# Performance work log

Hardware: AMD Instinct MI355X
Metric: run time of the kernel (lower is better)

## Reference

```python
import jax, jax.numpy as jnp
import numpy as np


def conv3d(x, w, b=None):
    # x: (N,C,D,H,W), w: (O,I,3,3,3), stride 1, padding 1 == SAME
    y = jax.lax.conv_general_dilated(x, w, (1, 1, 1), 'SAME',
                                     dimension_numbers=('NCDHW', 'OIDHW', 'NCDHW'))
    if b is not None:
        y = y + b[None, :, None, None, None]
    return y


def grid_sample_3d(vol, gx, gy, gz):
    # vol: (B,D,H,W); gx/gy/gz: normalized coords in [-1,1], shape (B,D,H,W)
    # trilinear, zeros padding, align_corners=True (old torch default)
    B, D, H, W = vol.shape
    ix = (gx + 1.0) * 0.5 * (W - 1)
    iy = (gy + 1.0) * 0.5 * (H - 1)
    iz = (gz + 1.0) * 0.5 * (D - 1)
    x0f, y0f, z0f = jnp.floor(ix), jnp.floor(iy), jnp.floor(iz)
    tx, ty, tz = ix - x0f, iy - y0f, iz - z0f
    x0 = x0f.astype(jnp.int32)
    y0 = y0f.astype(jnp.int32)
    z0 = z0f.astype(jnp.int32)
    vol_flat = vol.reshape(B, D * H * W)
    out = jnp.zeros_like(vol)
    for dz in (0, 1):
        for dy in (0, 1):
            for dx in (0, 1):
                xc, yc, zc = x0 + dx, y0 + dy, z0 + dz
                w = ((tx if dx else 1.0 - tx) * (ty if dy else 1.0 - ty)
                     * (tz if dz else 1.0 - tz))
                inb = ((xc >= 0) & (xc < W) & (yc >= 0) & (yc < H)
                       & (zc >= 0) & (zc < D))
                idx = ((jnp.clip(zc, 0, D - 1) * H + jnp.clip(yc, 0, H - 1)) * W
                       + jnp.clip(xc, 0, W - 1))
                val = jnp.take_along_axis(vol_flat, idx.reshape(B, -1), axis=1)
                val = val.reshape(B, D, H, W) * inb.astype(vol.dtype)
                out = out + w * val
    return out


def setup_inputs() -> dict:
    key = jax.random.key(0)
    k1, k2, k3, k4 = jax.random.split(key, 4)
    B, C, Cout, S = 2, 32, 64, 64
    x = jax.random.normal(k1, (B, C, S, S, S), dtype=jnp.float32)
    w_off = jax.random.normal(k2, (3 * C, C, 3, 3, 3), dtype=jnp.float32) * 0.0005
    w_reg = jax.random.normal(k3, (Cout, C, 3, 3, 3), dtype=jnp.float32) * 0.05
    b_reg = jax.random.normal(k4, (Cout,), dtype=jnp.float32) * 0.05
    return {"x": x, "w_off": w_off, "w_reg": w_reg, "b_reg": b_reg}


def reference(x, w_off, w_reg, b_reg):
    B, C, D, H, W = x.shape
    offset = conv3d(x, w_off)  # (B, 3C, D, H, W)
    off_w, off_h, _ = jnp.split(offset, 3, axis=1)
    # NOTE: original code has offset_d = offset_h (faithful bug)
    off_d = off_h
    off_w = off_w.reshape(B * C, D, H, W)
    off_h = off_h.reshape(B * C, D, H, W)
    off_d = off_d.reshape(B * C, D, H, W)
    # np.meshgrid default 'xy' indexing: shapes (H, W, D) -> requires D==H==W
    gw, gh, gd = np.meshgrid(np.linspace(-1, 1, W), np.linspace(-1, 1, H),
                             np.linspace(-1, 1, D))
    grid_w = jnp.asarray(gw, dtype=x.dtype)
    grid_h = jnp.asarray(gh, dtype=x.dtype)
    grid_d = jnp.asarray(gd, dtype=x.dtype)
    off_w = off_w + grid_w
    off_h = off_h + grid_h
    off_d = off_d + grid_d
    vol = x.reshape(B * C, D, H, W)
    # torch grid stack order: (offset_h, offset_w, offset_d) -> (x, y, z)
    sampled = grid_sample_3d(vol, off_h, off_w, off_d)
    sampled = sampled.reshape(B, C, D, H, W)
    return conv3d(sampled, w_reg, b_reg)
```

## Files before the change

### kernel.cpp

```cpp
#include <hip/hip_runtime.h>
#include <cstddef>

#define S 64
#define VOL (64*64*64)
#define CIN 32

typedef __attribute__((ext_vector_type(8))) short bf16x8;
typedef __attribute__((ext_vector_type(4))) float floatx4;

__device__ __forceinline__ unsigned short f2bf(float f) {
    union { float f; unsigned u; } v; v.f = f;
    unsigned r = v.u + 0x7fffu + ((v.u >> 16) & 1u);
    return (unsigned short)(r >> 16);
}
__device__ __forceinline__ float bf2f(unsigned short h) {
    union { unsigned u; float f; } v; v.u = ((unsigned)h) << 16;
    return v.f;
}
__device__ __forceinline__ int iclamp(int v, int lo, int hi) {
    return v < lo ? lo : (v > hi ? hi : v);
}

__device__ __forceinline__ void load4bf(const float* p, unsigned short* o) {
    const float4 v = *(const float4*)p;
    o[0] = f2bf(v.x); o[1] = f2bf(v.y); o[2] = f2bf(v.z); o[3] = f2bf(v.w);
}
__device__ __forceinline__ void load4bf(const unsigned short* p, unsigned short* o) {
    const ushort4 v = *(const ushort4*)p;
    o[0] = v.x; o[1] = v.y; o[2] = v.z; o[3] = v.w;
}

__global__ void prep_w_kernel(const float* __restrict__ w_off,
                              const float* __restrict__ w_reg,
                              unsigned short* __restrict__ wt1,
                              unsigned short* __restrict__ wt2) {
    int i = blockIdx.x * 256 + threadIdx.x;
    if (i >= 27 * 64 * 32) return;
    int ci = i & 31;
    int co = (i >> 5) & 63;
    int tap = i >> 11;
    wt1[i] = f2bf(w_off[(co * 32 + ci) * 27 + tap]);
    wt2[i] = f2bf(w_reg[(co * 32 + ci) * 27 + tap]);
}

template <typename TIN, bool WRITE_BF16>
__global__ __launch_bounds__(256, 2)
void conv_mfma_kernel(const TIN* __restrict__ src,
                      const unsigned short* __restrict__ wt,
                      const float* __restrict__ bias,
                      void* __restrict__ dstv) {
    __shared__ unsigned short lds[16 * 64 * 32];

    const int d0 = blockIdx.x * 2;
    const int h0 = blockIdx.y * 2;
    const int b  = blockIdx.z;
    const int t  = threadIdx.x;

    const TIN* sb = src + (size_t)b * CIN * VOL;

    const int w0 = (t & 15) << 2;
    const int c0 = (t >> 4) << 1;
    const int jj = c0 >> 3;
    const int cb = (c0 & 7) << 1;
    const int sw01 = (w0 >> 1) & 3;
    const int sw23 = ((w0 >> 1) + 1) & 3;

#pragma unroll
    for (int rr = 0; rr < 16; ++rr) {
        const int z = d0 - 1 + (rr >> 2);
        const int y = h0 - 1 + (rr & 3);
        unsigned pk0 = 0, pk1 = 0, pk2 = 0, pk3 = 0;
        if (((unsigned)z < 64u) && ((unsigned)y < 64u)) {
            const TIN* p0 = sb + (size_t)c0 * VOL + (z * 64 + y) * 64 + w0;
            unsigned short va[4], vb[4];
            load4bf(p0, va);
            load4bf(p0 + VOL, vb);
            pk0 = (unsigned)va[0] | ((unsigned)vb[0] << 16);
            pk1 = (unsigned)va[1] | ((unsigned)vb[1] << 16);
            pk2 = (unsigned)va[2] | ((unsigned)vb[2] << 16);
            pk3 = (unsigned)va[3] | ((unsigned)vb[3] << 16);
        }
        char* rbase = (char*)lds + (rr << 12) + cb;
        *(unsigned*)(rbase + ((w0 + 0) << 6) + ((jj ^ sw01) << 4)) = pk0;
        *(unsigned*)(rbase + ((w0 + 1) << 6) + ((jj ^ sw01) << 4)) = pk1;
        *(unsigned*)(rbase + ((w0 + 2) << 6) + ((jj ^ sw23) << 4)) = pk2;
        *(unsigned*)(rbase + ((w0 + 3) << 6) + ((jj ^ sw23) << 4)) = pk3;
    }
    __syncthreads();

    const int lane = t & 63;
    const int wv   = t >> 6;
    const int r    = lane & 15;
    const int q    = lane >> 4;
    const int dd   = wv >> 1;
    const int hh   = wv & 1;

    int P[4][3];
#pragma unroll
    for (int nt = 0; nt < 4; ++nt)
#pragma unroll
        for (int kw = 0; kw < 3; ++kw) {
            const int s  = nt * 16 + r + kw - 1;
            const int sc = s & 63;
            P[nt][kw] = (sc << 6) + ((q ^ ((sc >> 1) & 3)) << 4);
        }

    floatx4 acc[4][4];
#pragma unroll
    for (int mt = 0; mt < 4; ++mt)
#pragma unroll
        for (int nt = 0; nt < 4; ++nt)
#pragma unroll
            for (int rg = 0; rg < 4; ++rg) acc[mt][nt][rg] = 0.f;

    const bf16x8 z8 = {0, 0, 0, 0, 0, 0, 0, 0};

#pragma unroll
    for (int tap = 0; tap < 27; ++tap) {
        const int kd = tap / 9;
        const int kh = (tap % 9) / 3;
        const int kw = tap % 3;
        const int rowb = ((((dd + kd) << 2) + hh + kh) << 12);

        bf16x8 afr[4];
#pragma unroll
        for (int mt = 0; mt < 4; ++mt)
            afr[mt] = *(const bf16x8*)&wt[tap * 2048 + (mt * 16 + r) * 32 + q * 8];

        bf16x8 bfr[4];
#pragma unroll
        for (int nt = 0; nt < 4; ++nt)
            bfr[nt] = *(const bf16x8*)((const char*)lds + rowb + P[nt][kw]);

        if (kw == 0) { if (r == 0)  bfr[0] = z8; }
        if (kw == 2) { if (r == 15) bfr[3] = z8; }

#pragma unroll
        for (int mt = 0; mt < 4; ++mt)
#pragma unroll
            for (int nt = 0; nt < 4; ++nt)
                acc[mt][nt] = __builtin_amdgcn_mfma_f32_16x16x32_bf16(
                                  afr[mt], bfr[nt], acc[mt][nt], 0, 0, 0);
    }

    const int dw = (d0 + dd) * 4096 + (h0 + hh) * 64;
#pragma unroll
    for (int mt = 0; mt < 4; ++mt) {
#pragma unroll
        for (int nt = 0; nt < 4; ++nt) {
#pragma unroll
            for (int rg = 0; rg < 4; ++rg) {
                const int co  = mt * 16 + q * 4 + rg;
                const int pos = dw + nt * 16 + r;
                const size_t oidx = ((size_t)(b * 64 + co)) * VOL + pos;
                const float v = acc[mt][nt][rg];
                if (WRITE_BF16) {
                    ((unsigned short*)dstv)[oidx] = f2bf(v);
                } else {
                    ((float*)dstv)[oidx] = v + bias[co];
                }
            }
        }
    }
}

__global__ __launch_bounds__(256)
void gather_kernel(const float* __restrict__ x,
                   const unsigned short* __restrict__ off,
                   unsigned short* __restrict__ sampled) {
    __shared__ float res[16][17];

    const int bx = blockIdx.x;
    const int wt4 = bx & 3;
    const int dt  = (bx >> 2) & 3;
    const int h   = bx >> 4;
    const int c = blockIdx.y;
    const int b = blockIdx.z;
    const int t = threadIdx.x;
    const int d_i = t & 15;
    const int w_i = t >> 4;
    const int d = dt * 16 + d_i;
    const int w = wt4 * 16 + w_i;
    const int p = d * 4096 + h * 64 + w;

    const float* vol = x + ((size_t)(b * CIN + c)) * VOL;
    const float offw = bf2f(off[((size_t)(b * 64 + c)) * VOL + p]);
    const float offh = bf2f(off[((size_t)(b * 64 + 32 + c)) * VOL + p]);

    const float ix = offh * 31.5f + (float)d;
    const float iy = offw * 31.5f + (float)h;
    const float iz = offh * 31.5f + (float)w;

    const float x0f = floorf(ix), y0f = floorf(iy), z0f = floorf(iz);
    const float tx = ix - x0f, ty = iy - y0f, tz = iz - z0f;
    const int ix0 = (int)x0f, iy0 = (int)y0f, iz0 = (int)z0f;

    float out = 0.f;
#pragma unroll
    for (int dz = 0; dz < 2; ++dz) {
#pragma unroll
        for (int dy = 0; dy < 2; ++dy) {
#pragma unroll
            for (int dx = 0; dx < 2; ++dx) {
                const int xc = ix0 + dx, yc = iy0 + dy, zc = iz0 + dz;
                const bool inb = ((unsigned)xc < 64u) && ((unsigned)yc < 64u)
                              && ((unsigned)zc < 64u);
                const float wgt = (dx ? tx : 1.f - tx)
                                * (dy ? ty : 1.f - ty)
                                * (dz ? tz : 1.f - tz);
                const int xcc = iclamp(xc, 0, 63);
                const int ycc = iclamp(yc, 0, 63);
                const int zcc = iclamp(zc, 0, 63);
                const float val = vol[(zcc * 64 + ycc) * 64 + xcc];
                out += inb ? wgt * val : 0.f;
            }
        }
    }

    res[w_i][d_i] = out;
    __syncthreads();

    const int w_o = t & 15;
    const int d_o = t >> 4;
    sampled[((size_t)(b * CIN + c)) * VOL + (dt * 16 + d_o) * 4096 + h * 64
            + wt4 * 16 + w_o] = f2bf(res[w_o][d_o]);
}

extern "C" void kernel_launch(void* const* d_in, const int* in_sizes, int n_in,
                              void* d_out, int out_size, void* d_ws, size_t ws_size,
                              hipStream_t stream) {
    (void)in_sizes; (void)n_in; (void)out_size; (void)ws_size;
    const float* x     = (const float*)d_in[0];
    const float* w_off = (const float*)d_in[1];
    const float* w_reg = (const float*)d_in[2];
    const float* b_reg = (const float*)d_in[3];
    float* out = (float*)d_out;

    unsigned short* off     = (unsigned short*)d_ws;
    unsigned short* sampled = off + (size_t)2 * 64 * VOL;
    unsigned short* wt1     = sampled + (size_t)2 * CIN * VOL;
    unsigned short* wt2     = wt1 + 27 * 64 * 32;

    prep_w_kernel<<<216, 256, 0, stream>>>(w_off, w_reg, wt1, wt2);

    dim3 cgrid(32, 32, 2);
    conv_mfma_kernel<float, true><<<cgrid, 256, 0, stream>>>(x, wt1, nullptr, (void*)off);

    dim3 ggrid(1024, 32, 2);
    gather_kernel<<<ggrid, 256, 0, stream>>>(x, off, sampled);

    conv_mfma_kernel<unsigned short, false><<<cgrid, 256, 0, stream>>>(sampled, wt2, b_reg, (void*)out);
}
```

Measured before the change: 467.4 us.

## Pack offset pairs, remap gather grid per XCD, and load x-neighbors as pairs

Measured after the change: 426.2 us. -8.8%, faster.

```diff
diff --git a/kernel.cpp b/kernel.cpp
--- a/kernel.cpp
+++ b/kernel.cpp
@@ -7,6 +7,8 @@
 
 typedef __attribute__((ext_vector_type(8))) short bf16x8;
 typedef __attribute__((ext_vector_type(4))) float floatx4;
+
+struct __attribute__((packed, aligned(4))) fpair { float x, y; };
 
 __device__ __forceinline__ unsigned short f2bf(float f) {
     union { float f; unsigned u; } v; v.f = f;
@@ -43,7 +45,7 @@
     wt2[i] = f2bf(w_reg[(co * 32 + ci) * 27 + tap]);
 }
 
-template <typename TIN, bool WRITE_BF16>
+template <typename TIN, bool WRITE_OFF>
 __global__ __launch_bounds__(256, 2)
 void conv_mfma_kernel(const TIN* __restrict__ src,
                       const unsigned short* __restrict__ wt,
@@ -144,48 +146,74 @@
     }
 
     const int dw = (d0 + dd) * 4096 + (h0 + hh) * 64;
-#pragma unroll
-    for (int mt = 0; mt < 4; ++mt) {
-#pragma unroll
-        for (int nt = 0; nt < 4; ++nt) {
-#pragma unroll
-            for (int rg = 0; rg < 4; ++rg) {
-                const int co  = mt * 16 + q * 4 + rg;
-                const int pos = dw + nt * 16 + r;
-                const size_t oidx = ((size_t)(b * 64 + co)) * VOL + pos;
-                const float v = acc[mt][nt][rg];
-                if (WRITE_BF16) {
-                    ((unsigned short*)dstv)[oidx] = f2bf(v);
-                } else {
-                    ((float*)dstv)[oidx] = v + bias[co];
+    if (WRITE_OFF) {
+#pragma unroll
+        for (int mt = 0; mt < 2; ++mt) {
+#pragma unroll
+            for (int nt = 0; nt < 4; ++nt) {
+#pragma unroll
+                for (int rg = 0; rg < 4; ++rg) {
+                    const int c   = mt * 16 + q * 4 + rg;
+                    const int pos = dw + nt * 16 + r;
+                    const unsigned pk = (unsigned)f2bf(acc[mt][nt][rg])
+                                      | ((unsigned)f2bf(acc[mt + 2][nt][rg]) << 16);
+                    ((unsigned*)dstv)[((size_t)(b * 32 + c)) * VOL + pos] = pk;
                 }
             }
         }
+    } else {
+#pragma unroll
+        for (int mt = 0; mt < 4; ++mt) {
+#pragma unroll
+            for (int nt = 0; nt < 4; ++nt) {
+#pragma unroll
+                for (int rg = 0; rg < 4; ++rg) {
+                    const int co  = mt * 16 + q * 4 + rg;
+                    const int pos = dw + nt * 16 + r;
+                    ((float*)dstv)[((size_t)(b * 64 + co)) * VOL + pos]
+                        = acc[mt][nt][rg] + bias[co];
+                }
+            }
+        }
     }
 }
 
 __global__ __launch_bounds__(256)
 void gather_kernel(const float* __restrict__ x,
-                   const unsigned short* __restrict__ off,
+                   const unsigned* __restrict__ off32,
                    unsigned short* __restrict__ sampled) {
+    __shared__ unsigned ostage[16][17];
     __shared__ float res[16][17];
 
-    const int bx = blockIdx.x;
+    const unsigned gid = blockIdx.x;
+    const int xcd = gid & 7;
+    const int j   = gid >> 3;
+    const int v   = xcd + ((j >> 10) << 3);
+    const int bx  = j & 1023;
+    const int c   = v & 31;
+    const int b   = v >> 5;
     const int wt4 = bx & 3;
     const int dt  = (bx >> 2) & 3;
     const int h   = bx >> 4;
-    const int c = blockIdx.y;
-    const int b = blockIdx.z;
-    const int t = threadIdx.x;
+    const int t   = threadIdx.x;
+
+    {
+        const int wA = t & 15, dA = t >> 4;
+        ostage[dA][wA] = off32[((size_t)(b * 32 + c)) * VOL
+                               + (dt * 16 + dA) * 4096 + h * 64 + wt4 * 16 + wA];
+    }
+    __syncthreads();
+
     const int d_i = t & 15;
     const int w_i = t >> 4;
     const int d = dt * 16 + d_i;
     const int w = wt4 * 16 + w_i;
-    const int p = d * 4096 + h * 64 + w;
+
+    const unsigned ow = ostage[d_i][w_i];
+    const float offw = bf2f((unsigned short)(ow & 0xffffu));
+    const float offh = bf2f((unsigned short)(ow >> 16));
 
     const float* vol = x + ((size_t)(b * CIN + c)) * VOL;
-    const float offw = bf2f(off[((size_t)(b * 64 + c)) * VOL + p]);
-    const float offh = bf2f(off[((size_t)(b * 64 + 32 + c)) * VOL + p]);
 
     const float ix = offh * 31.5f + (float)d;
     const float iy = offw * 31.5f + (float)h;
@@ -195,25 +223,29 @@
     const float tx = ix - x0f, ty = iy - y0f, tz = iz - z0f;
     const int ix0 = (int)x0f, iy0 = (int)y0f, iz0 = (int)z0f;
 
+    const int bx0 = iclamp(ix0, 0, 62);
+    const bool sel = (ix0 == bx0);
+    const float w0x = ((unsigned)ix0 < 64u)       ? (1.f - tx) : 0.f;
+    const float w1x = ((unsigned)(ix0 + 1) < 64u) ? tx         : 0.f;
+
     float out = 0.f;
 #pragma unroll
     for (int dz = 0; dz < 2; ++dz) {
+        const int zc = iz0 + dz;
+        const bool zok = ((unsigned)zc < 64u);
+        const int zcc = iclamp(zc, 0, 63);
+        const float wz = dz ? tz : 1.f - tz;
 #pragma unroll
         for (int dy = 0; dy < 2; ++dy) {
-#pragma unroll
-            for (int dx = 0; dx < 2; ++dx) {
-                const int xc = ix0 + dx, yc = iy0 + dy, zc = iz0 + dz;
-                const bool inb = ((unsigned)xc < 64u) && ((unsigned)yc < 64u)
-                              && ((unsigned)zc < 64u);
-                const float wgt = (dx ? tx : 1.f - tx)
-                                * (dy ? ty : 1.f - ty)
-                                * (dz ? tz : 1.f - tz);
-                const int xcc = iclamp(xc, 0, 63);
-                const int ycc = iclamp(yc, 0, 63);
-                const int zcc = iclamp(zc, 0, 63);
-                const float val = vol[(zcc * 64 + ycc) * 64 + xcc];
-                out += inb ? wgt * val : 0.f;
-            }
+            const int yc = iy0 + dy;
+            const bool yok = ((unsigned)yc < 64u);
+            const int ycc = iclamp(yc, 0, 63);
+            const float wzy = (zok && yok) ? wz * (dy ? ty : 1.f - ty) : 0.f;
+
+            const fpair vp = *(const fpair*)&vol[(zcc * 64 + ycc) * 64 + bx0];
+            const float v0 = sel ? vp.x : vp.y;
+            const float v1 = sel ? vp.y : vp.x;
+            out += wzy * (w0x * v0 + w1x * v1);
         }
     }
 
@@ -236,18 +268,17 @@
     const float* b_reg = (const float*)d_in[3];
     float* out = (float*)d_out;
 
-    unsigned short* off     = (unsigned short*)d_ws;
-    unsigned short* sampled = off + (size_t)2 * 64 * VOL;
+    unsigned* off32         = (unsigned*)d_ws;
+    unsigned short* sampled = (unsigned short*)(off32 + (size_t)2 * 32 * VOL);
     unsigned short* wt1     = sampled + (size_t)2 * CIN * VOL;
     unsigned short* wt2     = wt1 + 27 * 64 * 32;
 
     prep_w_kernel<<<216, 256, 0, stream>>>(w_off, w_reg, wt1, wt2);
 
     dim3 cgrid(32, 32, 2);
-    conv_mfma_kernel<float, true><<<cgrid, 256, 0, stream>>>(x, wt1, nullptr, (void*)off);
-
-    dim3 ggrid(1024, 32, 2);
-    gather_kernel<<<ggrid, 256, 0, stream>>>(x, off, sampled);
+    conv_mfma_kernel<float, true><<<cgrid, 256, 0, stream>>>(x, wt1, nullptr, (void*)off32);
+
+    gather_kernel<<<65536, 256, 0, stream>>>(x, off32, sampled);
 
     conv_mfma_kernel<unsigned short, false><<<cgrid, 256, 0, stream>>>(sampled, wt2, b_reg, (void*)out);
 }
```
